# Kernel tuning notes

Measured on AMD Instinct MI355X. Metric: run time of the kernel, lower is better.

The kernel has to match this reference:

```python
import jax, jax.numpy as jnp
import numpy as np

N = 100000   # nodes
E = 600000   # edges
D_IN = 128
D_H = 128
D_OUT = 2


def setup_inputs() -> dict:
    key = jax.random.key(0)
    k0, k1, k2, k3 = jax.random.split(key, 4)
    x = jax.random.normal(k0, (N, D_IN), dtype=jnp.float32)
    edge_index = jax.random.randint(k1, (2, E), 0, N, dtype=jnp.int64)
    W1 = jax.random.normal(k2, (D_IN, D_H), dtype=jnp.float32) * (1.0 / np.sqrt(D_IN))
    b1 = jnp.zeros((D_H,), dtype=jnp.float32)
    W2 = jax.random.normal(k3, (D_H, D_OUT), dtype=jnp.float32) * (1.0 / np.sqrt(D_H))
    b2 = jnp.zeros((D_OUT,), dtype=jnp.float32)
    return {"x": x, "edge_index": edge_index, "W1": W1, "b1": b1, "W2": W2, "b2": b2}


def reference(x, edge_index, W1, b1, W2, b2):
    # 2-layer GCN (PyG GCNConv semantics): add self-loops, symmetric D^-1/2 A D^-1/2
    # normalization, linear transform, scatter-add aggregation at target nodes.
    # Dropout is identity in eval mode.
    n = x.shape[0]
    loop = jnp.arange(n)
    row = jnp.concatenate([edge_index[0], loop])  # message sources
    col = jnp.concatenate([edge_index[1], loop])  # aggregation targets
    ones = jnp.ones(row.shape[0], dtype=x.dtype)
    deg = jax.ops.segment_sum(ones, col, num_segments=n)
    dinv = jnp.where(deg > 0, jax.lax.rsqrt(deg), jnp.zeros_like(deg))
    norm = dinv[row] * dinv[col]  # [E+N]

    def conv(h, W, b):
        h = h @ W                         # [N, d_out]
        msg = h[row] * norm[:, None]      # gather + scale  [E+N, d_out]
        return jax.ops.segment_sum(msg, col, num_segments=n) + b

    h = jax.nn.relu(conv(x, W1, b1))
    return conv(h, W2, b2)
```

## Files before the change

kernel.cpp:

```cpp
#include <hip/hip_runtime.h>
#include <stdint.h>

#define N_NODES 100000
#define N_EDGES 600000
#define CAP 32

typedef __attribute__((ext_vector_type(8))) short bf16x8;
typedef __attribute__((ext_vector_type(4))) float f32x4;

__device__ __forceinline__ float bflo(unsigned int u) { return __uint_as_float(u << 16); }
__device__ __forceinline__ float bfhi(unsigned int u) { return __uint_as_float(u & 0xffff0000u); }
__device__ __forceinline__ unsigned int f2bf(float f) {
    unsigned int u = __float_as_uint(f);
    return (u + 0x7fffu + ((u >> 16) & 1u)) >> 16;
}

__global__ void k_pre(const float* __restrict__ W1, int* __restrict__ cnt,
                      unsigned short* __restrict__ W1f) {
    int b = blockIdx.x;
    if (b < 391) {
        int gid = b * 256 + threadIdx.x;
        cnt[gid] = 0;
        return;
    }
    int idx = (b - 391) * 256 + threadIdx.x;
    int t = idx >> 11;
    int k0c = (idx >> 9) & 3;
    int lane = (idx >> 3) & 63;
    int j = idx & 7;
    int n = t * 16 + (lane & 15);
    int k = k0c * 32 + (lane >> 4) * 8 + j;
    W1f[idx] = (unsigned short)f2bf(W1[k * 128 + n]);
}

__global__ __launch_bounds__(256) void k_fused(const float* __restrict__ x,
                                               const unsigned short* __restrict__ W1f,
                                               const int* __restrict__ ei,
                                               int* __restrict__ cnt,
                                               int* __restrict__ edata,
                                               unsigned short* __restrict__ h1b) {
    __shared__ unsigned short sxb[64][136];
    const int tid = threadIdx.x;
    const int b = blockIdx.x;
    if (b < 293) {
        int e0 = (b * 256 + tid) * 8;
        if (e0 + 8 <= N_EDGES) {
            int4 rA = *(const int4*)(ei + e0);
            int4 rB = *(const int4*)(ei + e0 + 4);
            int4 cA = *(const int4*)(ei + N_EDGES + e0);
            int4 cB = *(const int4*)(ei + N_EDGES + e0 + 4);
            int p0 = atomicAdd(&cnt[cA.x], 1);
            int p1 = atomicAdd(&cnt[cA.y], 1);
            int p2 = atomicAdd(&cnt[cA.z], 1);
            int p3 = atomicAdd(&cnt[cA.w], 1);
            int p4 = atomicAdd(&cnt[cB.x], 1);
            int p5 = atomicAdd(&cnt[cB.y], 1);
            int p6 = atomicAdd(&cnt[cB.z], 1);
            int p7 = atomicAdd(&cnt[cB.w], 1);
            if (p0 < CAP) edata[(size_t)cA.x * CAP + p0] = rA.x;
            if (p1 < CAP) edata[(size_t)cA.y * CAP + p1] = rA.y;
            if (p2 < CAP) edata[(size_t)cA.z * CAP + p2] = rA.z;
            if (p3 < CAP) edata[(size_t)cA.w * CAP + p3] = rA.w;
            if (p4 < CAP) edata[(size_t)cB.x * CAP + p4] = rB.x;
            if (p5 < CAP) edata[(size_t)cB.y * CAP + p5] = rB.y;
            if (p6 < CAP) edata[(size_t)cB.z * CAP + p6] = rB.z;
            if (p7 < CAP) edata[(size_t)cB.w * CAP + p7] = rB.w;
        }
        return;
    }
    const int rowBase = (b - 293) * 64;
#pragma unroll
    for (int i = 0; i < 8; i++) {
        int flat = tid + 256 * i;
        int row = flat >> 5;
        int f4 = flat & 31;
        int grow = rowBase + row;
        if (grow > N_NODES - 1) grow = N_NODES - 1;
        float4 v = *(const float4*)(x + (size_t)grow * 128 + f4 * 4);
        ushort4 p;
        p.x = (unsigned short)f2bf(v.x);
        p.y = (unsigned short)f2bf(v.y);
        p.z = (unsigned short)f2bf(v.z);
        p.w = (unsigned short)f2bf(v.w);
        *(ushort4*)(&sxb[row][f4 * 4]) = p;
    }
    __syncthreads();

    const int wv = tid >> 6;
    const int lane = tid & 63;
    const int l16 = lane & 15;
    const int quad = lane >> 4;
    const bf16x8* __restrict__ wf = (const bf16x8*)W1f;
    f32x4 acc[8];
#pragma unroll
    for (int t = 0; t < 8; t++) acc[t] = (f32x4){0.f, 0.f, 0.f, 0.f};

#pragma unroll
    for (int k0c = 0; k0c < 4; k0c++) {
        bf16x8 a = *(const bf16x8*)(&sxb[wv * 16 + l16][k0c * 32 + quad * 8]);
#pragma unroll
        for (int t = 0; t < 8; t++) {
            bf16x8 bfr = wf[(t * 4 + k0c) * 64 + lane];
            acc[t] = __builtin_amdgcn_mfma_f32_16x16x32_bf16(a, bfr, acc[t], 0, 0, 0);
        }
    }
    __syncthreads();
#pragma unroll
    for (int t = 0; t < 8; t++)
#pragma unroll
        for (int r = 0; r < 4; r++)
            sxb[wv * 16 + quad * 4 + r][t * 16 + l16] = (unsigned short)f2bf(acc[t][r]);
    __syncthreads();
#pragma unroll
    for (int i = 0; i < 4; i++) {
        int flat = tid + 256 * i;
        int row = flat >> 4;
        int c8 = flat & 15;
        int grow = rowBase + row;
        if (grow < N_NODES)
            *(uint4*)(h1b + (size_t)grow * 128 + c8 * 8) = *(const uint4*)(&sxb[row][c8 * 8]);
    }
}

__global__ __launch_bounds__(256) void k_agg1(const unsigned short* __restrict__ h1b,
                                              const int* __restrict__ edata,
                                              const int* __restrict__ cnt,
                                              const float* __restrict__ b1,
                                              const float* __restrict__ W2,
                                              float* __restrict__ h2) {
    int g = blockIdx.x * 256 + threadIdx.x;
    int wave = g >> 6;
    int lane = g & 63;
    int q = lane >> 4;
    int sub = lane & 15;
    int node = wave * 4 + q;
    int c0 = sub * 8;

    int c = cnt[node];
    int cc = (c < CAP) ? c : CAP;
    float d = rsqrtf((float)c + 1.0f);
    float d2 = d * d;
    uint4 us = *(const uint4*)(h1b + (size_t)node * 128 + c0);
    float a0 = bflo(us.x) * d2, a1 = bfhi(us.x) * d2;
    float a2 = bflo(us.y) * d2, a3 = bfhi(us.y) * d2;
    float a4 = bflo(us.z) * d2, a5 = bfhi(us.z) * d2;
    float a6 = bflo(us.w) * d2, a7 = bfhi(us.w) * d2;

    int cm = (cc < 16) ? cc : 16;
    int src_l = 0; float nrm_l = 0.0f;
    if (sub < cm) {
        src_l = edata[(size_t)node * CAP + sub];
        nrm_l = rsqrtf((float)cnt[src_l] + 1.0f) * d;
    }
    int base = q << 4;
    int i = 0;
    for (; i + 4 <= cm; i += 4) {
        int s0 = __shfl(src_l, base + i);
        int s1 = __shfl(src_l, base + i + 1);
        int s2 = __shfl(src_l, base + i + 2);
        int s3 = __shfl(src_l, base + i + 3);
        float n0 = __shfl(nrm_l, base + i);
        float n1 = __shfl(nrm_l, base + i + 1);
        float n2 = __shfl(nrm_l, base + i + 2);
        float n3 = __shfl(nrm_l, base + i + 3);
        uint4 u0 = *(const uint4*)(h1b + (size_t)s0 * 128 + c0);
        uint4 u1 = *(const uint4*)(h1b + (size_t)s1 * 128 + c0);
        uint4 u2 = *(const uint4*)(h1b + (size_t)s2 * 128 + c0);
        uint4 u3 = *(const uint4*)(h1b + (size_t)s3 * 128 + c0);
        a0 = fmaf(bflo(u0.x), n0, a0); a1 = fmaf(bfhi(u0.x), n0, a1);
        a2 = fmaf(bflo(u0.y), n0, a2); a3 = fmaf(bfhi(u0.y), n0, a3);
        a4 = fmaf(bflo(u0.z), n0, a4); a5 = fmaf(bfhi(u0.z), n0, a5);
        a6 = fmaf(bflo(u0.w), n0, a6); a7 = fmaf(bfhi(u0.w), n0, a7);
        a0 = fmaf(bflo(u1.x), n1, a0); a1 = fmaf(bfhi(u1.x), n1, a1);
        a2 = fmaf(bflo(u1.y), n1, a2); a3 = fmaf(bfhi(u1.y), n1, a3);
        a4 = fmaf(bflo(u1.z), n1, a4); a5 = fmaf(bfhi(u1.z), n1, a5);
        a6 = fmaf(bflo(u1.w), n1, a6); a7 = fmaf(bfhi(u1.w), n1, a7);
        a0 = fmaf(bflo(u2.x), n2, a0); a1 = fmaf(bfhi(u2.x), n2, a1);
        a2 = fmaf(bflo(u2.y), n2, a2); a3 = fmaf(bfhi(u2.y), n2, a3);
        a4 = fmaf(bflo(u2.z), n2, a4); a5 = fmaf(bfhi(u2.z), n2, a5);
        a6 = fmaf(bflo(u2.w), n2, a6); a7 = fmaf(bfhi(u2.w), n2, a7);
        a0 = fmaf(bflo(u3.x), n3, a0); a1 = fmaf(bfhi(u3.x), n3, a1);
        a2 = fmaf(bflo(u3.y), n3, a2); a3 = fmaf(bfhi(u3.y), n3, a3);
        a4 = fmaf(bflo(u3.z), n3, a4); a5 = fmaf(bfhi(u3.z), n3, a5);
        a6 = fmaf(bflo(u3.w), n3, a6); a7 = fmaf(bfhi(u3.w), n3, a7);
    }
    for (; i < cm; i++) {
        int s = __shfl(src_l, base + i);
        float n = __shfl(nrm_l, base + i);
        uint4 u = *(const uint4*)(h1b + (size_t)s * 128 + c0);
        a0 = fmaf(bflo(u.x), n, a0); a1 = fmaf(bfhi(u.x), n, a1);
        a2 = fmaf(bflo(u.y), n, a2); a3 = fmaf(bfhi(u.y), n, a3);
        a4 = fmaf(bflo(u.z), n, a4); a5 = fmaf(bfhi(u.z), n, a5);
        a6 = fmaf(bflo(u.w), n, a6); a7 = fmaf(bfhi(u.w), n, a7);
    }
    for (; i < cc; i++) {
        int s = edata[(size_t)node * CAP + i];
        float n = rsqrtf((float)cnt[s] + 1.0f) * d;
        uint4 u = *(const uint4*)(h1b + (size_t)s * 128 + c0);
        a0 = fmaf(bflo(u.x), n, a0); a1 = fmaf(bfhi(u.x), n, a1);
        a2 = fmaf(bflo(u.y), n, a2); a3 = fmaf(bfhi(u.y), n, a3);
        a4 = fmaf(bflo(u.z), n, a4); a5 = fmaf(bfhi(u.z), n, a5);
        a6 = fmaf(bflo(u.w), n, a6); a7 = fmaf(bfhi(u.w), n, a7);
    }

    float4 bbA = *(const float4*)(b1 + c0);
    float4 bbB = *(const float4*)(b1 + c0 + 4);
    float v0 = fmaxf(a0 + bbA.x, 0.0f);
    float v1 = fmaxf(a1 + bbA.y, 0.0f);
    float v2 = fmaxf(a2 + bbA.z, 0.0f);
    float v3 = fmaxf(a3 + bbA.w, 0.0f);
    float v4 = fmaxf(a4 + bbB.x, 0.0f);
    float v5 = fmaxf(a5 + bbB.y, 0.0f);
    float v6 = fmaxf(a6 + bbB.z, 0.0f);
    float v7 = fmaxf(a7 + bbB.w, 0.0f);
    float4 wA = *(const float4*)(W2 + c0 * 2);
    float4 wB = *(const float4*)(W2 + c0 * 2 + 4);
    float4 wC = *(const float4*)(W2 + c0 * 2 + 8);
    float4 wD = *(const float4*)(W2 + c0 * 2 + 12);
    float p0 = v0 * wA.x + v1 * wA.z + v2 * wB.x + v3 * wB.z
             + v4 * wC.x + v5 * wC.z + v6 * wD.x + v7 * wD.z;
    float p1 = v0 * wA.y + v1 * wA.w + v2 * wB.y + v3 * wB.w
             + v4 * wC.y + v5 * wC.w + v6 * wD.y + v7 * wD.w;
    for (int offl = 8; offl; offl >>= 1) {
        p0 += __shfl_xor(p0, offl);
        p1 += __shfl_xor(p1, offl);
    }
    if (sub == 0) *(float2*)(h2 + (size_t)node * 2) = make_float2(p0, p1);
}

__global__ void k_agg2(const float* __restrict__ h2, const int* __restrict__ edata,
                       const int* __restrict__ cnt, const float* __restrict__ b2,
                       float* __restrict__ out) {
    int n = blockIdx.x * 256 + threadIdx.x;
    if (n >= N_NODES) return;
    int c = cnt[n];
    int cc = (c < CAP) ? c : CAP;
    float d = rsqrtf((float)c + 1.0f);
    float d2 = d * d;
    float2 h = *(const float2*)(h2 + (size_t)n * 2);
    float o0 = h.x * d2, o1 = h.y * d2;
    for (int i = 0; i < cc; i++) {
        int src = edata[(size_t)n * CAP + i];
        float nrm = rsqrtf((float)cnt[src] + 1.0f) * d;
        float2 v = *(const float2*)(h2 + (size_t)src * 2);
        o0 = fmaf(v.x, nrm, o0);
        o1 = fmaf(v.y, nrm, o1);
    }
    *(float2*)(out + (size_t)n * 2) = make_float2(o0 + b2[0], o1 + b2[1]);
}

extern "C" void kernel_launch(void* const* d_in, const int* in_sizes, int n_in,
                              void* d_out, int out_size, void* d_ws, size_t ws_size,
                              hipStream_t stream) {
    const float* x  = (const float*)d_in[0];
    const int* ei   = (const int*)d_in[1];
    const float* W1 = (const float*)d_in[2];
    const float* b1 = (const float*)d_in[3];
    const float* W2 = (const float*)d_in[4];
    const float* b2 = (const float*)d_in[5];
    float* out = (float*)d_out;

    char* w = (char*)d_ws;
    int*   cnt   = (int*)w;                     w += 100096 * 4;
    int*   edata = (int*)w;                     w += (size_t)N_NODES * CAP * 4;
    unsigned short* h1b = (unsigned short*)w;   w += (size_t)N_NODES * 128 * 2;
    float* h2    = (float*)w;                   w += (size_t)N_NODES * 2 * 4;
    unsigned short* W1f = (unsigned short*)w;

    k_pre  <<<455, 256, 0, stream>>>(W1, cnt, W1f);
    k_fused<<<1856, 256, 0, stream>>>(x, W1f, ei, cnt, edata, h1b);
    k_agg1 <<<6250, 256, 0, stream>>>(h1b, edata, cnt, b1, W2, h2);
    k_agg2 <<<391, 256, 0, stream>>>(h2, edata, cnt, b2, out);
}
```

Baseline: 173.0 us.

## Pre-scale layer-2 features by source norm and split agg2 across two lanes

In k_agg1, the layer-2 features are now multiplied by the node's d factor before being stored. This lets k_agg2 skip the per-edge lookup of cnt[src] and its rsqrt, and apply the target's d once at the end. Each node in k_agg2 is now handled by two lanes that split the edge list and combine their sums with a shuffle, doubling the grid. The inner loop is also unrolled by two to put more gathers in flight. Risk: this relies on `d` already being in scope in k_agg1, which is not visible.

```diff
diff --git a/kernel.cpp b/kernel.cpp
--- a/kernel.cpp
+++ b/kernel.cpp
@@ -225,28 +225,45 @@
         p0 += __shfl_xor(p0, offl);
         p1 += __shfl_xor(p1, offl);
     }
-    if (sub == 0) *(float2*)(h2 + (size_t)node * 2) = make_float2(p0, p1);
-}
-
-__global__ void k_agg2(const float* __restrict__ h2, const int* __restrict__ edata,
-                       const int* __restrict__ cnt, const float* __restrict__ b2,
-                       float* __restrict__ out) {
-    int n = blockIdx.x * 256 + threadIdx.x;
+    if (sub == 0) *(float2*)(h2 + (size_t)node * 2) = make_float2(d * p0, d * p1);
+}
+
+__global__ __launch_bounds__(256) void k_agg2(const float* __restrict__ h2p,
+                                              const int* __restrict__ edata,
+                                              const int* __restrict__ cnt,
+                                              const float* __restrict__ b2,
+                                              float* __restrict__ out) {
+    int gid = blockIdx.x * 256 + threadIdx.x;
+    int n = gid >> 1;
+    int half = gid & 1;
     if (n >= N_NODES) return;
     int c = cnt[n];
     int cc = (c < CAP) ? c : CAP;
-    float d = rsqrtf((float)c + 1.0f);
-    float d2 = d * d;
-    float2 h = *(const float2*)(h2 + (size_t)n * 2);
-    float o0 = h.x * d2, o1 = h.y * d2;
-    for (int i = 0; i < cc; i++) {
-        int src = edata[(size_t)n * CAP + i];
-        float nrm = rsqrtf((float)cnt[src] + 1.0f) * d;
-        float2 v = *(const float2*)(h2 + (size_t)src * 2);
-        o0 = fmaf(v.x, nrm, o0);
-        o1 = fmaf(v.y, nrm, o1);
-    }
-    *(float2*)(out + (size_t)n * 2) = make_float2(o0 + b2[0], o1 + b2[1]);
+    const int* eb = edata + (size_t)n * CAP;
+    float o0 = 0.f, o1 = 0.f;
+    int i = half;
+    for (; i + 2 < cc; i += 4) {
+        int s0 = eb[i];
+        int s1 = eb[i + 2];
+        float2 v0 = *(const float2*)(h2p + (size_t)s0 * 2);
+        float2 v1 = *(const float2*)(h2p + (size_t)s1 * 2);
+        o0 += v0.x + v1.x;
+        o1 += v0.y + v1.y;
+    }
+    for (; i < cc; i += 2) {
+        int s = eb[i];
+        float2 v = *(const float2*)(h2p + (size_t)s * 2);
+        o0 += v.x;
+        o1 += v.y;
+    }
+    o0 += __shfl_xor(o0, 1);
+    o1 += __shfl_xor(o1, 1);
+    if (half == 0) {
+        float d = rsqrtf((float)c + 1.0f);
+        float2 h = *(const float2*)(h2p + (size_t)n * 2);
+        *(float2*)(out + (size_t)n * 2) =
+            make_float2(d * (h.x + o0) + b2[0], d * (h.y + o1) + b2[1]);
+    }
 }
 
 extern "C" void kernel_launch(void* const* d_in, const int* in_sizes, int n_in,
@@ -270,5 +287,5 @@
     k_pre  <<<455, 256, 0, stream>>>(W1, cnt, W1f);
     k_fused<<<1856, 256, 0, stream>>>(x, W1f, ei, cnt, edata, h1b);
     k_agg1 <<<6250, 256, 0, stream>>>(h1b, edata, cnt, b1, W2, h2);
-    k_agg2 <<<391, 256, 0, stream>>>(h2, edata, cnt, b2, out);
-}
+    k_agg2 <<<782, 256, 0, stream>>>(h2, edata, cnt, b2, out);
+}
```

Measured after the change: 169.5 us. 1.02x faster.
